# Performance work log

Measured on AMD Instinct MI355X. Metric: run time of the kernel, lower is better.

Reference implementation:

```python
import jax, jax.numpy as jnp
import numpy as np

B, T, H = 2, 2048, 1024
NUM_HEADS = 16
HEAD_DIM = H // NUM_HEADS
MAX_REL = 4


def setup_inputs() -> dict:
    key = jax.random.key(0)
    ks = jax.random.split(key, 12)
    s = 1.0 / np.sqrt(H)
    inp = {
        "x": jax.random.normal(ks[0], (B, T, H), dtype=jnp.float32),
        "text_mask": jax.random.randint(ks[1], (B, T), 0, 2, dtype=jnp.int32),
        "Wq": jax.random.normal(ks[2], (H, H), dtype=jnp.float32) * s,
        "bq": jnp.zeros((H,), dtype=jnp.float32),
        "Wk": jax.random.normal(ks[3], (H, H), dtype=jnp.float32) * s,
        "bk": jnp.zeros((H,), dtype=jnp.float32),
        "Wv": jax.random.normal(ks[4], (H, H), dtype=jnp.float32) * s,
        "bv": jnp.zeros((H,), dtype=jnp.float32),
        "Wo": jax.random.normal(ks[5], (H, H), dtype=jnp.float32) * s,
        "bo": jnp.zeros((H,), dtype=jnp.float32),
        "rel_bias": jax.random.normal(ks[6], (2 * MAX_REL + 1, NUM_HEADS), dtype=jnp.float32),
    }
    return inp


def reference(x, text_mask, Wq, bq, Wk, bk, Wv, bv, Wo, bo, rel_bias):
    b, t, h = x.shape
    scale = HEAD_DIM ** (-0.5)

    def proj(W, bias):
        # [b,t,h] -> [b,heads,t,head_dim]
        return (x @ W.T + bias).reshape(b, t, NUM_HEADS, HEAD_DIM).transpose(0, 2, 1, 3)

    q = proj(Wq, bq)
    k = proj(Wk, bk)
    v = proj(Wv, bv)

    scores = jnp.einsum("bhqd,bhkd->bhqk", q, k) * scale  # [b,heads,t,t]

    pos = jnp.arange(t)
    rel = jnp.clip(pos[None, :] - pos[:, None], -MAX_REL, MAX_REL) + MAX_REL  # [t,t]
    bias = rel_bias[rel]  # [t,t,heads]
    scores = scores + bias.transpose(2, 0, 1)[None]  # broadcast over batch

    key_valid = text_mask.astype(bool)  # [b,t]
    scores = jnp.where(key_valid[:, None, None, :], scores, -10000.0)

    attn = jax.nn.softmax(scores, axis=-1)
    hidden = jnp.einsum("bhqk,bhkd->bhqd", attn, v)
    hidden = hidden.transpose(0, 2, 1, 3).reshape(b, t, h)
    out = hidden @ Wo.T + bo
    return out * text_mask.astype(out.dtype)[:, :, None]
```

## Files before the change

kernel.cpp:

```cpp
#include <hip/hip_runtime.h>
#include <hip/hip_bf16.h>

#define B_ 2
#define T_ 2048
#define H_ 1024
#define NH 16
#define HD 64

typedef __attribute__((ext_vector_type(8))) short bf16x8;
typedef __attribute__((ext_vector_type(4))) short bf16x4;
typedef __attribute__((ext_vector_type(4))) float f32x4;

#define ASYNC_COPY16(gptr, lptr)                                              \
    __builtin_amdgcn_global_load_lds(                                         \
        (const __attribute__((address_space(1))) void*)(gptr),                \
        (__attribute__((address_space(3))) void*)(lptr), 16, 0, 0)

#if __has_builtin(__builtin_amdgcn_exp2f)
#define EXP2(x) __builtin_amdgcn_exp2f(x)
#else
static __device__ inline float EXP2(float x) {
    float r;
    asm volatile("v_exp_f32 %0, %1" : "=v"(r) : "v"(x));
    return r;
}
#endif

static __device__ inline unsigned short f2bf(float f) {
    union { float f; unsigned u; } v; v.f = f;
    unsigned r = v.u + 0x7fff + ((v.u >> 16) & 1);
    return (unsigned short)(r >> 16);
}

static __device__ inline unsigned pkbf(float a, float b) {
    float2 t2; t2.x = a; t2.y = b;
    __hip_bfloat162 h = __float22bfloat162_rn(t2);
    union { __hip_bfloat162 h; unsigned u; } cv; cv.h = h;
    return cv.u;
}

static __device__ inline bf16x4 mk4(unsigned lo, unsigned hi) {
    union { bf16x4 v; unsigned u[2]; } cv;
    cv.u[0] = lo; cv.u[1] = hi;
    return cv.v;
}

static __device__ inline f32x4 zero4() {
    f32x4 z = {0.f, 0.f, 0.f, 0.f};
    return z;
}

#define LOG2E 1.44269504088896f

__global__ void cvt_kernel(const float* __restrict__ x,
                           const float* __restrict__ wq,
                           const float* __restrict__ wk,
                           const float* __restrict__ wv,
                           const float* __restrict__ wo,
                           const int* __restrict__ maskp,
                           unsigned short* __restrict__ dst,
                           unsigned* __restrict__ cidx,
                           unsigned short* __restrict__ vidx,
                           unsigned short* __restrict__ maskc,
                           unsigned* __restrict__ meta,
                           float* __restrict__ outz) {
    if (blockIdx.x > 8192) {
        long long idx =
            ((long long)(blockIdx.x - 8193) * 256 + threadIdx.x) * 4;
        if (idx < 4194304LL) {
            float4 z = {0.f, 0.f, 0.f, 0.f};
            *(float4*)(outz + idx) = z;
        }
        return;
    }
    if (blockIdx.x == 8192) {
        __shared__ unsigned ps[256];
        int t = threadIdx.x;
        int base = t * 16;
        int bb = base >> 11;
        unsigned mv = 0, cnt = 0;
#pragma unroll
        for (int i = 0; i < 16; i++) {
            if (maskp[base + i]) { mv |= (1u << i); cnt++; }
        }
        ps[t] = cnt;
        __syncthreads();
        for (int off = 1; off < 128; off <<= 1) {
            unsigned add = ((t & 127) >= off) ? ps[t - off] : 0;
            __syncthreads();
            ps[t] += add;
            __syncthreads();
        }
        unsigned cnt0 = ps[127], cnt1 = ps[255];
        unsigned ex = ps[t] - cnt;
        unsigned local = ex;
        unsigned g = (bb ? cnt0 : 0) + ex;
        for (int i = 0; i < 16; i++) {
            if (mv & (1u << i)) {
                cidx[g] = (unsigned)(base + i);
                vidx[bb * 2048 + local] =
                    (unsigned short)(base + i - bb * 2048);
                maskc[bb * 2048 + local] = 0x3F80;
                g++; local++;
            }
        }
        if (t == 0) { meta[0] = cnt0; meta[1] = cnt1; meta[2] = cnt0 + cnt1; }
        __syncthreads();
        unsigned C = cnt0 + cnt1;
        for (unsigned i = C + t; i < 4224; i += 256) cidx[i] = 0;
        for (unsigned i = cnt0 + t; i < 2048; i += 256) {
            vidx[i] = 0; maskc[i] = 0;
        }
        for (unsigned i = cnt1 + t; i < 2048; i += 256) {
            vidx[2048 + i] = 0; maskc[2048 + i] = 0;
        }
        return;
    }
    long long i0 = ((long long)blockIdx.x * blockDim.x + threadIdx.x) * 4;
    const float* src; long long off;
    if (i0 < 4194304LL)      { src = x;  off = i0; }
    else if (i0 < 5242880LL) { src = wq; off = i0 - 4194304LL; }
    else if (i0 < 6291456LL) { src = wk; off = i0 - 5242880LL; }
    else if (i0 < 7340032LL) { src = wv; off = i0 - 6291456LL; }
    else                     { src = wo; off = i0 - 7340032LL; }
    float4 f = *(const float4*)(src + off);
    ushort4 o;
    o.x = f2bf(f.x); o.y = f2bf(f.y); o.z = f2bf(f.z); o.w = f2bf(f.w);
    *(ushort4*)(dst + i0) = o;
}

__global__ __launch_bounds__(256) void qkv_gemm(
    const unsigned short* __restrict__ A,
    const unsigned short* __restrict__ Bm,
    const float* __restrict__ bq, const float* __restrict__ bk,
    const float* __restrict__ bv,
    const unsigned* __restrict__ cidx, const unsigned* __restrict__ meta,
    unsigned short* __restrict__ qout, unsigned short* __restrict__ kout,
    unsigned short* __restrict__ vout) {
    const int K = 1024;
    int C  = (int)meta[2];
    int c0 = (int)meta[0];
    int m0 = blockIdx.y * 64, n0 = blockIdx.x * 128;
    if (m0 >= C) return;
    __shared__ __align__(16) unsigned short As[64 * 32];
    __shared__ __align__(16) unsigned short Bs[128 * 32];
    int t = threadIdx.x;
    int w = t >> 6, lane = t & 63;
    int wm = (w >> 1) * 32, wn = (w & 1) * 64;
    int c = lane & 15, qd = lane >> 4;

    f32x4 acc[2][4];
#pragma unroll
    for (int i = 0; i < 2; i++)
#pragma unroll
        for (int j = 0; j < 4; j++) acc[i][j] = zero4();

    int srow = t >> 2, sseg = (t & 3) * 8;
    int r1 = (int)cidx[m0 + srow];
    const unsigned short* ag1 = A + (long long)r1 * K + sseg;
    const unsigned short* bg1 = Bm + (long long)(n0 + srow) * K + sseg;
    const unsigned short* bg2 = bg1 + 64LL * K;
    unsigned short* la1 = As + t * 8;
    unsigned short* lb1 = Bs + t * 8;
    unsigned short* lb2 = Bs + (t + 256) * 8;

    for (int kk = 0; kk < K; kk += 32) {
        __syncthreads();
        ASYNC_COPY16(ag1 + kk, la1);
        ASYNC_COPY16(bg1 + kk, lb1);
        ASYNC_COPY16(bg2 + kk, lb2);
        __syncthreads();
        bf16x8 af[2], bf[4];
#pragma unroll
        for (int i = 0; i < 2; i++)
            af[i] = *(const bf16x8*)(As + (wm + i * 16 + c) * 32 + qd * 8);
#pragma unroll
        for (int j = 0; j < 4; j++)
            bf[j] = *(const bf16x8*)(Bs + (wn + j * 16 + c) * 32 + qd * 8);
#pragma unroll
        for (int i = 0; i < 2; i++)
#pragma unroll
            for (int j = 0; j < 4; j++)
                acc[i][j] = __builtin_amdgcn_mfma_f32_16x16x32_bf16(
                    af[i], bf[j], acc[i][j], 0, 0, 0);
    }

    int gr[2][4];
#pragma unroll
    for (int i = 0; i < 2; i++)
#pragma unroll
        for (int r = 0; r < 4; r++) {
            int m = m0 + wm + i * 16 + qd * 4 + r;
            gr[i][r] = (m < C) ? (int)cidx[m] : -1;
        }

    const float QSCALE = 0.125f * LOG2E;
#pragma unroll
    for (int i = 0; i < 2; i++) {
        int m_base = m0 + wm + i * 16 + qd * 4;
#pragma unroll
        for (int j = 0; j < 4; j++) {
            int n = n0 + wn + j * 16 + c;
            int sel = n >> 10, within = n & 1023;
            int head = within >> 6, d = within & 63;
            if (sel == 0) {
                float ba = bq[within];
#pragma unroll
                for (int r = 0; r < 4; r++) {
                    if (gr[i][r] >= 0) {
                        int bb = gr[i][r] >> 11;
                        int loc = (m_base + r) - (bb ? c0 : 0);
                        qout[(((long long)(bb * NH + head)) * T_ + loc) * HD +
                             d] = f2bf((acc[i][j][r] + ba) * QSCALE);
                    }
                }
            } else if (sel == 1) {
                float ba = bk[within];
#pragma unroll
                for (int r = 0; r < 4; r++) {
                    if (gr[i][r] >= 0) {
                        int bb = gr[i][r] >> 11;
                        int loc = (m_base + r) - (bb ? c0 : 0);
                        kout[(((long long)(bb * NH + head)) * T_ + loc) * HD +
                             d] = f2bf(acc[i][j][r] + ba);
                    }
                }
            } else {
                float ba = bv[within];
                int g0 = gr[i][0], g3 = gr[i][3];
                int bb0 = g0 >> 11;
                int loc0 = m_base - (bb0 ? c0 : 0);
                if (g3 >= 0 && bb0 == (g3 >> 11) && ((loc0 & 3) == 0)) {
                    uint2 ov;
                    ov.x = pkbf(acc[i][j][0] + ba, acc[i][j][1] + ba);
                    ov.y = pkbf(acc[i][j][2] + ba, acc[i][j][3] + ba);
                    *(uint2*)(vout +
                              (((long long)(bb0 * NH + head)) * HD + d) * T_ +
                              loc0) = ov;
                } else {
#pragma unroll
                    for (int r = 0; r < 4; r++) {
                        if (gr[i][r] >= 0) {
                            int bb = gr[i][r] >> 11;
                            int loc = (m_base + r) - (bb ? c0 : 0);
                            vout[(((long long)(bb * NH + head)) * HD + d) *
                                     T_ +
                                 loc] = f2bf(acc[i][j][r] + ba);
                        }
                    }
                }
            }
        }
    }
}

__global__ __launch_bounds__(256) void out_gemm(
    const unsigned short* __restrict__ A,
    const unsigned short* __restrict__ Bm,
    const float* __restrict__ bo,
    const unsigned* __restrict__ cidx, const unsigned* __restrict__ meta,
    float* __restrict__ out) {
    const int K = 1024;
    int C = (int)meta[2];
    int m0 = blockIdx.y * 64, n0 = blockIdx.x * 64;
    if (m0 >= C) return;
    __shared__ __align__(16) unsigned short As[64 * 32];
    __shared__ __align__(16) unsigned short Bs[64 * 32];
    int t = threadIdx.x;
    int w = t >> 6, lane = t & 63;
    int wm = (w >> 1) * 32, wn = (w & 1) * 32;
    int c = lane & 15, qd = lane >> 4;

    f32x4 acc[2][2];
#pragma unroll
    for (int i = 0; i < 2; i++)
#pragma unroll
        for (int j = 0; j < 2; j++) acc[i][j] = zero4();

    int srow = t >> 2, sseg = (t & 3) * 8;
    int r1 = (int)cidx[m0 + srow];
    const unsigned short* ag1 = A + (long long)r1 * K + sseg;
    const unsigned short* bg1 = Bm + (long long)(n0 + srow) * K + sseg;
    unsigned short* la1 = As + t * 8;
    unsigned short* lb1 = Bs + t * 8;

    for (int kk = 0; kk < K; kk += 32) {
        __syncthreads();
        ASYNC_COPY16(ag1 + kk, la1);
        ASYNC_COPY16(bg1 + kk, lb1);
        __syncthreads();
        bf16x8 af[2], bf[2];
#pragma unroll
        for (int i = 0; i < 2; i++)
            af[i] = *(const bf16x8*)(As + (wm + i * 16 + c) * 32 + qd * 8);
#pragma unroll
        for (int j = 0; j < 2; j++)
            bf[j] = *(const bf16x8*)(Bs + (wn + j * 16 + c) * 32 + qd * 8);
#pragma unroll
        for (int i = 0; i < 2; i++)
#pragma unroll
            for (int j = 0; j < 2; j++)
                acc[i][j] = __builtin_amdgcn_mfma_f32_16x16x32_bf16(
                    af[i], bf[j], acc[i][j], 0, 0, 0);
    }

#pragma unroll
    for (int i = 0; i < 2; i++) {
#pragma unroll
        for (int r = 0; r < 4; r++) {
            int m = m0 + wm + i * 16 + qd * 4 + r;
            if (m < C) {
                long long g = (long long)cidx[m];
#pragma unroll
                for (int j = 0; j < 2; j++) {
                    int n = n0 + wn + j * 16 + c;
                    out[g * 1024 + n] = acc[i][j][r] + bo[n];
                }
            }
        }
    }
}

__global__ __launch_bounds__(256, 2) void attn_kernel(
    const unsigned short* __restrict__ qg,
    const unsigned short* __restrict__ kg,
    const unsigned short* __restrict__ vTg,
    const float* __restrict__ rel_bias,
    const unsigned short* __restrict__ maskc,
    const unsigned short* __restrict__ vidxg,
    const unsigned* __restrict__ meta,
    unsigned short* __restrict__ hid) {
    int hb = blockIdx.x, qt = blockIdx.y;
    int h = hb & 15, b = hb >> 4;
    int cnt = (int)meta[b];
    if (qt * 128 >= cnt) return;
    int nkt = (cnt + 63) >> 6;
    int t = threadIdx.x, w = t >> 6, lane = t & 63;
    int c = lane & 15, qd = lane >> 4;

    __shared__ __align__(16) unsigned short lk[2][64 * 72];
    __shared__ __align__(16) unsigned short lvT[2][64 * 72];
    __shared__ __align__(16) unsigned short lmk[2][64];
    __shared__ __align__(16) unsigned short lki[2][64];
    __shared__ float lrbf[16];

    if (t < 9) lrbf[t] = rel_bias[t * 16 + h] * LOG2E;
    float rb0 = rel_bias[0 * 16 + h] * LOG2E;
    float rb8 = rel_bias[8 * 16 + h] * LOG2E;

    const unsigned short* qp =
        qg + (((long long)(b * NH + h)) * T_ + qt * 128) * HD;
    const unsigned short* kp = kg + ((long long)(b * NH + h)) * T_ * HD;
    const unsigned short* vp = vTg + ((long long)(b * NH + h)) * HD * T_;

    bf16x8 qf[2][2];
#pragma unroll
    for (int mt = 0; mt < 2; mt++)
#pragma unroll
        for (int ks = 0; ks < 2; ks++)
            qf[mt][ks] = *(const bf16x8*)(qp + (w * 32 + mt * 16 + c) * HD +
                                          ks * 32 + qd * 8);

    const int imin = qt * 128 + w * 32;
    int imin_t = (int)vidxg[b * 2048 + min(imin, cnt - 1)];
    int imax_t = (int)vidxg[b * 2048 + min(imin + 31, cnt - 1)];
    int itrue[2];
#pragma unroll
    for (int mt = 0; mt < 2; mt++)
        itrue[mt] =
            (int)vidxg[b * 2048 + min(imin + mt * 16 + c, cnt - 1)];

    f32x4 o[4][2];
    f32x4 lacc[2];
#pragma unroll
    for (int dt = 0; dt < 4; dt++)
#pragma unroll
        for (int mt = 0; mt < 2; mt++) o[dt][mt] = zero4();
    lacc[0] = zero4(); lacc[1] = zero4();

    int srow = t >> 2, sseg = (t & 3) * 16;
    const unsigned short* kst = kp + srow * HD + sseg;
    const unsigned short* vst = vp + srow * T_ + sseg;
    const unsigned short* mst = maskc + b * 2048 + t;
    const unsigned short* ist = vidxg + b * 2048 + t * 8;

    uint4 rk0 = *(const uint4*)(kst);
    uint4 rk1 = *(const uint4*)(kst + 8);
    uint4 rv0 = *(const uint4*)(vst);
    uint4 rv1 = *(const uint4*)(vst + 8);
    unsigned short rm = (t < 64) ? *mst : 0;
    uint4 rki = {0, 0, 0, 0};
    if (t < 8) rki = *(const uint4*)(ist);

    for (int kt = 0; kt < nkt; kt++) {
        unsigned short* KB = lk[kt & 1];
        unsigned short* VB = lvT[kt & 1];
        unsigned short* MK = lmk[kt & 1];
        unsigned short* KI = lki[kt & 1];
        *(uint4*)(KB + srow * 72 + sseg)     = rk0;
        *(uint4*)(KB + srow * 72 + sseg + 8) = rk1;
        *(uint4*)(VB + srow * 72 + sseg)     = rv0;
        *(uint4*)(VB + srow * 72 + sseg + 8) = rv1;
        if (t < 64) MK[t] = rm;
        if (t < 8) *(uint4*)(KI + t * 8) = rki;
        {
            int ktn = (kt < nkt - 1) ? kt + 1 : nkt - 1;
            rk0 = *(const uint4*)(kst + ktn * 64 * HD);
            rk1 = *(const uint4*)(kst + ktn * 64 * HD + 8);
            rv0 = *(const uint4*)(vst + ktn * 64);
            rv1 = *(const uint4*)(vst + ktn * 64 + 8);
            if (t < 64) rm = mst[ktn * 64];
            if (t < 8) rki = *(const uint4*)(ist + ktn * 64);
        }
        __syncthreads();

        int j0 = kt * 64;
        int jlo_t = (int)KI[0];
        int jhi_t = (int)KI[min(63, cnt - 1 - j0)];
        bool far_lo = (jhi_t <= imin_t - 4);
        bool far_hi = (jlo_t >= imax_t + 4);
        float ub = far_lo ? rb0 : rb8;
        bool nearband = !(far_lo || far_hi);

#pragma unroll
        for (int jt = 0; jt < 4; jt++) {
            bf16x8 kf0 = *(const bf16x8*)(KB + (jt * 16 + c) * 72 + qd * 8);
            bf16x8 kf1 =
                *(const bf16x8*)(KB + (jt * 16 + c) * 72 + 32 + qd * 8);
            bf16x4 vld4 = *(const bf16x4*)(MK + jt * 16 + qd * 4);
            ushort4 kiv = *(const ushort4*)(KI + jt * 16 + qd * 4);
            bf16x4 vf[4];
#pragma unroll
            for (int dt = 0; dt < 4; dt++)
                vf[dt] = *(const bf16x4*)(VB + (dt * 16 + c) * 72 + jt * 16 +
                                          qd * 4);
#pragma unroll
            for (int mt = 0; mt < 2; mt++) {
                f32x4 acc = zero4();
                acc = __builtin_amdgcn_mfma_f32_16x16x32_bf16(kf0, qf[mt][0],
                                                              acc, 0, 0, 0);
                acc = __builtin_amdgcn_mfma_f32_16x16x32_bf16(kf1, qf[mt][1],
                                                              acc, 0, 0, 0);
                float p0, p1, p2, p3;
                if (nearband) {
                    int it = itrue[mt];
                    int r0 = (int)kiv.x - it;
                    r0 = r0 < -4 ? -4 : (r0 > 4 ? 4 : r0);
                    int r1 = (int)kiv.y - it;
                    r1 = r1 < -4 ? -4 : (r1 > 4 ? 4 : r1);
                    int r2 = (int)kiv.z - it;
                    r2 = r2 < -4 ? -4 : (r2 > 4 ? 4 : r2);
                    int r3 = (int)kiv.w - it;
                    r3 = r3 < -4 ? -4 : (r3 > 4 ? 4 : r3);
                    p0 = EXP2(acc[0] + lrbf[r0 + 4]);
                    p1 = EXP2(acc[1] + lrbf[r1 + 4]);
                    p2 = EXP2(acc[2] + lrbf[r2 + 4]);
                    p3 = EXP2(acc[3] + lrbf[r3 + 4]);
                } else {
                    p0 = EXP2(acc[0] + ub);
                    p1 = EXP2(acc[1] + ub);
                    p2 = EXP2(acc[2] + ub);
                    p3 = EXP2(acc[3] + ub);
                }
                bf16x4 pfrag = mk4(pkbf(p0, p1), pkbf(p2, p3));
                lacc[mt] = __builtin_amdgcn_mfma_f32_16x16x16bf16_1k(
                    vld4, pfrag, lacc[mt], 0, 0, 0);
#pragma unroll
                for (int dt = 0; dt < 4; dt++)
                    o[dt][mt] = __builtin_amdgcn_mfma_f32_16x16x16bf16_1k(
                        vf[dt], pfrag, o[dt][mt], 0, 0, 0);
            }
        }
    }

#pragma unroll
    for (int mt = 0; mt < 2; mt++) {
        int rc = imin + mt * 16 + c;
        if (rc < cnt) {
            float invl = 1.0f / lacc[mt][0];
            long long row = (long long)b * T_ + itrue[mt];
#pragma unroll
            for (int dt = 0; dt < 4; dt++) {
                uint2 ov;
                ov.x = pkbf(o[dt][mt][0] * invl, o[dt][mt][1] * invl);
                ov.y = pkbf(o[dt][mt][2] * invl, o[dt][mt][3] * invl);
                *(uint2*)(hid + row * H_ + h * HD + dt * 16 + qd * 4) = ov;
            }
        }
    }
}

extern "C" void kernel_launch(void* const* d_in, const int* in_sizes, int n_in,
                              void* d_out, int out_size, void* d_ws,
                              size_t ws_size, hipStream_t stream) {
    const float* x    = (const float*)d_in[0];
    const int* maskp  = (const int*)d_in[1];
    const float* Wq   = (const float*)d_in[2];
    const float* bq   = (const float*)d_in[3];
    const float* Wk   = (const float*)d_in[4];
    const float* bk   = (const float*)d_in[5];
    const float* Wv   = (const float*)d_in[6];
    const float* bv   = (const float*)d_in[7];
    const float* Wo   = (const float*)d_in[8];
    const float* bo   = (const float*)d_in[9];
    const float* rb   = (const float*)d_in[10];
    float* out        = (float*)d_out;

    unsigned short* ws = (unsigned short*)d_ws;
    unsigned short* xb    = ws;
    unsigned short* wqkv  = ws + 4194304LL;
    unsigned short* wo_b  = ws + 7340032LL;
    unsigned short* qb    = ws + 8388608LL;
    unsigned short* kb    = ws + 12582912LL;
    unsigned short* vTb   = ws + 16777216LL;
    unsigned short* hid   = ws + 20971520LL;
    unsigned* meta        = (unsigned*)(ws + 25165824LL);
    unsigned* cidx        = (unsigned*)(ws + 25165856LL);
    unsigned short* vidx  = ws + 25174304LL;
    unsigned short* maskc = ws + 25178400LL;

    cvt_kernel<<<12289, 256, 0, stream>>>(x, Wq, Wk, Wv, Wo, maskp, ws, cidx,
                                          vidx, maskc, meta, out);
    qkv_gemm<<<dim3(24, 64), 256, 0, stream>>>(xb, wqkv, bq, bk, bv, cidx,
                                               meta, qb, kb, vTb);
    attn_kernel<<<dim3(32, 16), 256, 0, stream>>>(qb, kb, vTb, rb, maskc,
                                                  vidx, meta, hid);
    out_gemm<<<dim3(16, 64), 256, 0, stream>>>(hid, wo_b, bo, cidx, meta,
                                               out);
}
```

Measured before the change: 181.2 us.

## Enlarge GEMM tiles and switch attention PV to 16x16x32 MFMA with permuted K rows

The QKV GEMM tile grows from 64x128 to 128x128 and the output GEMM tile from 64x64 to 64x128, so each block does more MFMAs per LDS load and fewer blocks are launched. The attention kernel now handles 32 keys per step. K rows are permuted on load so the two QK^T results pack straight into an 8-wide bf16 P fragment, which lets the PV and row-sum products use the K=32 MFMA instead of the K=16 one. The costs are higher register pressure and fewer blocks (lower occupancy), and the row permutation has to match the mask and index layout exactly.

```diff
diff --git a/kernel.cpp b/kernel.cpp
--- a/kernel.cpp
+++ b/kernel.cpp
@@ -39,9 +39,10 @@
     return cv.u;
 }
 
-static __device__ inline bf16x4 mk4(unsigned lo, unsigned hi) {
-    union { bf16x4 v; unsigned u[2]; } cv;
-    cv.u[0] = lo; cv.u[1] = hi;
+static __device__ inline bf16x8 mk8(unsigned a, unsigned b, unsigned c,
+                                    unsigned d) {
+    union { bf16x8 v; unsigned u[4]; } cv;
+    cv.u[0] = a; cv.u[1] = b; cv.u[2] = c; cv.u[3] = d;
     return cv.v;
 }
 
@@ -140,54 +141,58 @@
     const int K = 1024;
     int C  = (int)meta[2];
     int c0 = (int)meta[0];
-    int m0 = blockIdx.y * 64, n0 = blockIdx.x * 128;
+    int m0 = blockIdx.y * 128, n0 = blockIdx.x * 128;
     if (m0 >= C) return;
-    __shared__ __align__(16) unsigned short As[64 * 32];
+    __shared__ __align__(16) unsigned short As[128 * 32];
     __shared__ __align__(16) unsigned short Bs[128 * 32];
     int t = threadIdx.x;
     int w = t >> 6, lane = t & 63;
-    int wm = (w >> 1) * 32, wn = (w & 1) * 64;
+    int wm = (w >> 1) * 64, wn = (w & 1) * 64;
     int c = lane & 15, qd = lane >> 4;
 
-    f32x4 acc[2][4];
-#pragma unroll
-    for (int i = 0; i < 2; i++)
+    f32x4 acc[4][4];
+#pragma unroll
+    for (int i = 0; i < 4; i++)
 #pragma unroll
         for (int j = 0; j < 4; j++) acc[i][j] = zero4();
 
     int srow = t >> 2, sseg = (t & 3) * 8;
     int r1 = (int)cidx[m0 + srow];
+    int r2 = (int)cidx[m0 + 64 + srow];
     const unsigned short* ag1 = A + (long long)r1 * K + sseg;
+    const unsigned short* ag2 = A + (long long)r2 * K + sseg;
     const unsigned short* bg1 = Bm + (long long)(n0 + srow) * K + sseg;
     const unsigned short* bg2 = bg1 + 64LL * K;
     unsigned short* la1 = As + t * 8;
+    unsigned short* la2 = As + (t + 256) * 8;
     unsigned short* lb1 = Bs + t * 8;
     unsigned short* lb2 = Bs + (t + 256) * 8;
 
     for (int kk = 0; kk < K; kk += 32) {
         __syncthreads();
         ASYNC_COPY16(ag1 + kk, la1);
+        ASYNC_COPY16(ag2 + kk, la2);
         ASYNC_COPY16(bg1 + kk, lb1);
         ASYNC_COPY16(bg2 + kk, lb2);
         __syncthreads();
-        bf16x8 af[2], bf[4];
-#pragma unroll
-        for (int i = 0; i < 2; i++)
+        bf16x8 af[4], bf[4];
+#pragma unroll
+        for (int i = 0; i < 4; i++)
             af[i] = *(const bf16x8*)(As + (wm + i * 16 + c) * 32 + qd * 8);
 #pragma unroll
         for (int j = 0; j < 4; j++)
             bf[j] = *(const bf16x8*)(Bs + (wn + j * 16 + c) * 32 + qd * 8);
 #pragma unroll
-        for (int i = 0; i < 2; i++)
+        for (int i = 0; i < 4; i++)
 #pragma unroll
             for (int j = 0; j < 4; j++)
                 acc[i][j] = __builtin_amdgcn_mfma_f32_16x16x32_bf16(
                     af[i], bf[j], acc[i][j], 0, 0, 0);
     }
 
-    int gr[2][4];
-#pragma unroll
-    for (int i = 0; i < 2; i++)
+    int gr[4][4];
+#pragma unroll
+    for (int i = 0; i < 4; i++)
 #pragma unroll
         for (int r = 0; r < 4; r++) {
             int m = m0 + wm + i * 16 + qd * 4 + r;
@@ -196,7 +201,7 @@
 
     const float QSCALE = 0.125f * LOG2E;
 #pragma unroll
-    for (int i = 0; i < 2; i++) {
+    for (int i = 0; i < 4; i++) {
         int m_base = m0 + wm + i * 16 + qd * 4;
 #pragma unroll
         for (int j = 0; j < 4; j++) {
@@ -262,44 +267,47 @@
     float* __restrict__ out) {
     const int K = 1024;
     int C = (int)meta[2];
-    int m0 = blockIdx.y * 64, n0 = blockIdx.x * 64;
+    int m0 = blockIdx.y * 64, n0 = blockIdx.x * 128;
     if (m0 >= C) return;
     __shared__ __align__(16) unsigned short As[64 * 32];
-    __shared__ __align__(16) unsigned short Bs[64 * 32];
+    __shared__ __align__(16) unsigned short Bs[128 * 32];
     int t = threadIdx.x;
     int w = t >> 6, lane = t & 63;
-    int wm = (w >> 1) * 32, wn = (w & 1) * 32;
+    int wm = (w >> 1) * 32, wn = (w & 1) * 64;
     int c = lane & 15, qd = lane >> 4;
 
-    f32x4 acc[2][2];
+    f32x4 acc[2][4];
 #pragma unroll
     for (int i = 0; i < 2; i++)
 #pragma unroll
-        for (int j = 0; j < 2; j++) acc[i][j] = zero4();
+        for (int j = 0; j < 4; j++) acc[i][j] = zero4();
 
     int srow = t >> 2, sseg = (t & 3) * 8;
     int r1 = (int)cidx[m0 + srow];
     const unsigned short* ag1 = A + (long long)r1 * K + sseg;
     const unsigned short* bg1 = Bm + (long long)(n0 + srow) * K + sseg;
+    const unsigned short* bg2 = bg1 + 64LL * K;
     unsigned short* la1 = As + t * 8;
     unsigned short* lb1 = Bs + t * 8;
+    unsigned short* lb2 = Bs + (t + 256) * 8;
 
     for (int kk = 0; kk < K; kk += 32) {
         __syncthreads();
         ASYNC_COPY16(ag1 + kk, la1);
         ASYNC_COPY16(bg1 + kk, lb1);
-        __syncthreads();
-        bf16x8 af[2], bf[2];
+        ASYNC_COPY16(bg2 + kk, lb2);
+        __syncthreads();
+        bf16x8 af[2], bf[4];
 #pragma unroll
         for (int i = 0; i < 2; i++)
             af[i] = *(const bf16x8*)(As + (wm + i * 16 + c) * 32 + qd * 8);
 #pragma unroll
-        for (int j = 0; j < 2; j++)
+        for (int j = 0; j < 4; j++)
             bf[j] = *(const bf16x8*)(Bs + (wn + j * 16 + c) * 32 + qd * 8);
 #pragma unroll
         for (int i = 0; i < 2; i++)
 #pragma unroll
-            for (int j = 0; j < 2; j++)
+            for (int j = 0; j < 4; j++)
                 acc[i][j] = __builtin_amdgcn_mfma_f32_16x16x32_bf16(
                     af[i], bf[j], acc[i][j], 0, 0, 0);
     }
@@ -312,7 +320,7 @@
             if (m < C) {
                 long long g = (long long)cidx[m];
 #pragma unroll
-                for (int j = 0; j < 2; j++) {
+                for (int j = 0; j < 4; j++) {
                     int n = n0 + wn + j * 16 + c;
                     out[g * 1024 + n] = acc[i][j][r] + bo[n];
                 }
@@ -379,7 +387,9 @@
     lacc[0] = zero4(); lacc[1] = zero4();
 
     int srow = t >> 2, sseg = (t & 3) * 16;
-    const unsigned short* kst = kp + srow * HD + sseg;
+    int rr = srow & 15, hf = (srow >> 4) & 1;
+    int gk = (srow & 32) + (rr >> 2) * 8 + hf * 4 + (rr & 3);
+    const unsigned short* kst = kp + gk * HD + sseg;
     const unsigned short* vst = vp + srow * T_ + sseg;
     const unsigned short* mst = maskc + b * 2048 + t;
     const unsigned short* ist = vidxg + b * 2048 + t * 8;
@@ -423,52 +433,77 @@
         bool nearband = !(far_lo || far_hi);
 
 #pragma unroll
-        for (int jt = 0; jt < 4; jt++) {
-            bf16x8 kf0 = *(const bf16x8*)(KB + (jt * 16 + c) * 72 + qd * 8);
-            bf16x8 kf1 =
-                *(const bf16x8*)(KB + (jt * 16 + c) * 72 + 32 + qd * 8);
-            bf16x4 vld4 = *(const bf16x4*)(MK + jt * 16 + qd * 4);
-            ushort4 kiv = *(const ushort4*)(KI + jt * 16 + qd * 4);
-            bf16x4 vf[4];
+        for (int jp = 0; jp < 2; jp++) {
+            int jb = jp * 32;
+            const unsigned short* kbase = KB + (jb + c) * 72 + qd * 8;
+            bf16x8 kfA0 = *(const bf16x8*)(kbase);
+            bf16x8 kfA1 = *(const bf16x8*)(kbase + 32);
+            bf16x8 kfB0 = *(const bf16x8*)(kbase + 16 * 72);
+            bf16x8 kfB1 = *(const bf16x8*)(kbase + 16 * 72 + 32);
+            bf16x8 m8 = *(const bf16x8*)(MK + jb + qd * 8);
+            ushort4 kivA = *(const ushort4*)(KI + jb + qd * 8);
+            ushort4 kivB = *(const ushort4*)(KI + jb + qd * 8 + 4);
+            bf16x8 vf[4];
 #pragma unroll
             for (int dt = 0; dt < 4; dt++)
-                vf[dt] = *(const bf16x4*)(VB + (dt * 16 + c) * 72 + jt * 16 +
-                                          qd * 4);
+                vf[dt] = *(const bf16x8*)(VB + (dt * 16 + c) * 72 + jb +
+                                          qd * 8);
 #pragma unroll
             for (int mt = 0; mt < 2; mt++) {
-                f32x4 acc = zero4();
-                acc = __builtin_amdgcn_mfma_f32_16x16x32_bf16(kf0, qf[mt][0],
-                                                              acc, 0, 0, 0);
-                acc = __builtin_amdgcn_mfma_f32_16x16x32_bf16(kf1, qf[mt][1],
-                                                              acc, 0, 0, 0);
-                float p0, p1, p2, p3;
+                f32x4 accA = zero4(), accB = zero4();
+                accA = __builtin_amdgcn_mfma_f32_16x16x32_bf16(
+                    kfA0, qf[mt][0], accA, 0, 0, 0);
+                accA = __builtin_amdgcn_mfma_f32_16x16x32_bf16(
+                    kfA1, qf[mt][1], accA, 0, 0, 0);
+                accB = __builtin_amdgcn_mfma_f32_16x16x32_bf16(
+                    kfB0, qf[mt][0], accB, 0, 0, 0);
+                accB = __builtin_amdgcn_mfma_f32_16x16x32_bf16(
+                    kfB1, qf[mt][1], accB, 0, 0, 0);
+                float pA0, pA1, pA2, pA3, pB0, pB1, pB2, pB3;
                 if (nearband) {
                     int it = itrue[mt];
-                    int r0 = (int)kiv.x - it;
-                    r0 = r0 < -4 ? -4 : (r0 > 4 ? 4 : r0);
-                    int r1 = (int)kiv.y - it;
-                    r1 = r1 < -4 ? -4 : (r1 > 4 ? 4 : r1);
-                    int r2 = (int)kiv.z - it;
-                    r2 = r2 < -4 ? -4 : (r2 > 4 ? 4 : r2);
-                    int r3 = (int)kiv.w - it;
-                    r3 = r3 < -4 ? -4 : (r3 > 4 ? 4 : r3);
-                    p0 = EXP2(acc[0] + lrbf[r0 + 4]);
-                    p1 = EXP2(acc[1] + lrbf[r1 + 4]);
-                    p2 = EXP2(acc[2] + lrbf[r2 + 4]);
-                    p3 = EXP2(acc[3] + lrbf[r3 + 4]);
+                    int a0 = (int)kivA.x - it;
+                    a0 = a0 < -4 ? -4 : (a0 > 4 ? 4 : a0);
+                    int a1 = (int)kivA.y - it;
+                    a1 = a1 < -4 ? -4 : (a1 > 4 ? 4 : a1);
+                    int a2 = (int)kivA.z - it;
+                    a2 = a2 < -4 ? -4 : (a2 > 4 ? 4 : a2);
+                    int a3 = (int)kivA.w - it;
+                    a3 = a3 < -4 ? -4 : (a3 > 4 ? 4 : a3);
+                    int b0i = (int)kivB.x - it;
+                    b0i = b0i < -4 ? -4 : (b0i > 4 ? 4 : b0i);
+                    int b1i = (int)kivB.y - it;
+                    b1i = b1i < -4 ? -4 : (b1i > 4 ? 4 : b1i);
+                    int b2i = (int)kivB.z - it;
+                    b2i = b2i < -4 ? -4 : (b2i > 4 ? 4 : b2i);
+                    int b3i = (int)kivB.w - it;
+                    b3i = b3i < -4 ? -4 : (b3i > 4 ? 4 : b3i);
+                    pA0 = EXP2(accA[0] + lrbf[a0 + 4]);
+                    pA1 = EXP2(accA[1] + lrbf[a1 + 4]);
+                    pA2 = EXP2(accA[2] + lrbf[a2 + 4]);
+                    pA3 = EXP2(accA[3] + lrbf[a3 + 4]);
+                    pB0 = EXP2(accB[0] + lrbf[b0i + 4]);
+                    pB1 = EXP2(accB[1] + lrbf[b1i + 4]);
+                    pB2 = EXP2(accB[2] + lrbf[b2i + 4]);
+                    pB3 = EXP2(accB[3] + lrbf[b3i + 4]);
                 } else {
-                    p0 = EXP2(acc[0] + ub);
-                    p1 = EXP2(acc[1] + ub);
-                    p2 = EXP2(acc[2] + ub);
-                    p3 = EXP2(acc[3] + ub);
+                    pA0 = EXP2(accA[0] + ub);
+                    pA1 = EXP2(accA[1] + ub);
+                    pA2 = EXP2(accA[2] + ub);
+                    pA3 = EXP2(accA[3] + ub);
+                    pB0 = EXP2(accB[0] + ub);
+                    pB1 = EXP2(accB[1] + ub);
+                    pB2 = EXP2(accB[2] + ub);
+                    pB3 = EXP2(accB[3] + ub);
                 }
-                bf16x4 pfrag = mk4(pkbf(p0, p1), pkbf(p2, p3));
-                lacc[mt] = __builtin_amdgcn_mfma_f32_16x16x16bf16_1k(
-                    vld4, pfrag, lacc[mt], 0, 0, 0);
+                bf16x8 pf = mk8(pkbf(pA0, pA1), pkbf(pA2, pA3),
+                                pkbf(pB0, pB1), pkbf(pB2, pB3));
+                lacc[mt] = __builtin_amdgcn_mfma_f32_16x16x32_bf16(
+                    m8, pf, lacc[mt], 0, 0, 0);
 #pragma unroll
                 for (int dt = 0; dt < 4; dt++)
-                    o[dt][mt] = __builtin_amdgcn_mfma_f32_16x16x16bf16_1k(
-                        vf[dt], pfrag, o[dt][mt], 0, 0, 0);
+                    o[dt][mt] = __builtin_amdgcn_mfma_f32_16x16x32_bf16(
+                        vf[dt], pf, o[dt][mt], 0, 0, 0);
             }
         }
     }
@@ -521,10 +556,10 @@
 
     cvt_kernel<<<12289, 256, 0, stream>>>(x, Wq, Wk, Wv, Wo, maskp, ws, cidx,
                                           vidx, maskc, meta, out);
-    qkv_gemm<<<dim3(24, 64), 256, 0, stream>>>(xb, wqkv, bq, bk, bv, cidx,
+    qkv_gemm<<<dim3(24, 32), 256, 0, stream>>>(xb, wqkv, bq, bk, bv, cidx,
                                                meta, qb, kb, vTb);
     attn_kernel<<<dim3(32, 16), 256, 0, stream>>>(qb, kb, vTb, rb, maskc,
                                                   vidx, meta, hid);
-    out_gemm<<<dim3(16, 64), 256, 0, stream>>>(hid, wo_b, bo, cidx, meta,
-                                               out);
-}
+    out_gemm<<<dim3(8, 64), 256, 0, stream>>>(hid, wo_b, bo, cidx, meta,
+                                              out);
+}
```

Result: slower. 188.9 us (+4.3%).
